# Kernel tuning notes

Hardware: AMD Instinct MI355X
Metric: run time of the kernel (lower is better)

The kernel has to match this reference:

```python
import jax, jax.numpy as jnp
import numpy as np

DIM = 1024
INNER = int(DIM * 1.5)
EPS = 1e-6


def setup_inputs() -> dict:
    key = jax.random.key(0)
    ks = jax.random.split(key, 8)
    B, L, D = 4, 2048, DIM
    s1 = 1.0 / np.sqrt(D)
    s2 = 1.0 / np.sqrt(INNER)
    return {
        "x": jax.random.normal(ks[0], (B, L, D), jnp.float32),
        "W1": jax.random.normal(ks[1], (D, INNER), jnp.float32) * s1,
        "b1": jnp.zeros((INNER,), jnp.float32),
        "W2": jax.random.normal(ks[2], (INNER, 3 * D), jnp.float32) * s2,
        "b2": jnp.zeros((3 * D,), jnp.float32),
        "Wv": jax.random.normal(ks[3], (D, D), jnp.float32) * (0.5 * s1),
        "bv": jnp.zeros((D,), jnp.float32),
        "mix_weight": jnp.full((D,), 0.5, jnp.float32),
        "norm_weight": jnp.ones((D,), jnp.float32),
    }


def rmsnorm(x, w):
    norm = jnp.sqrt(jnp.mean(x * x, axis=-1, keepdims=True) + EPS)
    return x / norm * w


def reference(x, W1, b1, W2, b2, Wv, bv, mix_weight, norm_weight):
    B, L, D = x.shape
    h = jax.nn.silu(x @ W1 + b1)              # [B,L,inner]
    qkg = h @ W2 + b2                          # [B,L,3D]
    q, k, g = jnp.split(qkg, 3, axis=-1)
    scores = jnp.einsum('bld,bmd->blm', q, k) / jnp.sqrt(jnp.float32(D))
    attn = jax.nn.softmax(scores, axis=-1)
    v = (x @ Wv + bv) * jax.nn.sigmoid(g)      # gated values [B,L,D]
    global_info = jnp.einsum('blm,bmd->bld', attn, v)
    output = mix_weight * global_info + (1.0 - mix_weight) * x
    return rmsnorm(output, norm_weight)
```

## Files before the change

kernel.cpp:

```cpp
#include <hip/hip_runtime.h>
#include <hip/hip_bf16.h>
#include <stdint.h>


typedef __bf16 bf16x8 __attribute__((ext_vector_type(8)));
typedef float f32x4 __attribute__((ext_vector_type(4)));

__device__ __forceinline__ unsigned short f2bf(float f) {
    unsigned int u = __float_as_uint(f);
    u += 0x7fffu + ((u >> 16) & 1u);
    return (unsigned short)(u >> 16);
}
__device__ __forceinline__ float bf2f(unsigned short s) {
    return __uint_as_float(((unsigned int)s) << 16);
}
__device__ __forceinline__ void llds16(const void* g, void* l) {
    __builtin_amdgcn_global_load_lds(
        (const __attribute__((address_space(1))) void*)g,
        (__attribute__((address_space(3))) void*)l, 16, 0, 0);
}

__global__ __launch_bounds__(256) void cvt_f32_bf16(
    const float* __restrict__ in, unsigned short* __restrict__ out, long long n8) {
    long long i = (long long)blockIdx.x * 256 + threadIdx.x;
    if (i >= n8) return;
    float4 a = ((const float4*)in)[2 * i];
    float4 b = ((const float4*)in)[2 * i + 1];
    ushort4 p0, p1;
    p0.x = f2bf(a.x); p0.y = f2bf(a.y); p0.z = f2bf(a.z); p0.w = f2bf(a.w);
    p1.x = f2bf(b.x); p1.y = f2bf(b.y); p1.z = f2bf(b.z); p1.w = f2bf(b.w);
    ((ushort4*)out)[2 * i] = p0;
    ((ushort4*)out)[2 * i + 1] = p1;
}

__global__ __launch_bounds__(256) void transpose_cvt(
    const float* __restrict__ in, unsigned short* __restrict__ out, int R, int C) {
    __shared__ unsigned short tile[32][33];
    int c0 = blockIdx.x * 32, r0 = blockIdx.y * 32;
    int cc = threadIdx.x & 31, rr = threadIdx.x >> 5;
#pragma unroll
    for (int p = 0; p < 4; ++p) {
        int r = rr + p * 8;
        tile[r][cc] = f2bf(in[(size_t)(r0 + r) * C + c0 + cc]);
    }
    __syncthreads();
#pragma unroll
    for (int p = 0; p < 4; ++p) {
        int c = rr + p * 8;
        out[(size_t)(c0 + c) * R + r0 + cc] = tile[cc][c];
    }
}

__global__ __launch_bounds__(256) void transpose_v(
    const unsigned short* __restrict__ in, unsigned short* __restrict__ out) {
    __shared__ unsigned short tile[32][33];
    int d0 = blockIdx.x * 32, m0 = blockIdx.y * 32;
    int cc = threadIdx.x & 31, rr = threadIdx.x >> 5;
#pragma unroll
    for (int p = 0; p < 4; ++p) {
        int r = rr + p * 8;
        tile[r][cc] = in[(size_t)(m0 + r) * 1024 + d0 + cc];
    }
    __syncthreads();
    int b = m0 >> 11, l0 = m0 & 2047;
#pragma unroll
    for (int p = 0; p < 4; ++p) {
        int d = rr + p * 8;
        out[((size_t)b * 1024 + d0 + d) * 2048 + l0 + cc] = tile[cc][d];
    }
}

template <int EPI>
__global__ __launch_bounds__(256, 3) void gemmk(
    const unsigned short* __restrict__ A, int lda, long long Abs,
    const unsigned short* __restrict__ B, int ldb, long long Bbs,
    int K,
    void* __restrict__ out, int ldo, long long Obs,
    const float* __restrict__ bias,
    const unsigned short* __restrict__ gate, int ldg,
    const float* __restrict__ xres, const float* __restrict__ mix,
    float scale, int gx) {
    __shared__ unsigned short lds[24576];
    const int tid = threadIdx.x, lane = tid & 63, wid = tid >> 6;
    const int nwg = gridDim.x;
    const int bswz = ((int)blockIdx.x & 7) * (nwg >> 3) + ((int)blockIdx.x >> 3);
    const int bx = bswz % gx, by = bswz / gx;
    const int bm = by * 128, bn = bx * 128;
    const int z = blockIdx.z;
    A += (long long)z * Abs;
    B += (long long)z * Bbs;
    const int NT = K >> 5;

    const int srow = tid >> 2;
    const int sswz = ((tid & 3) ^ ((tid >> 3) & 3)) * 8;
    size_t ag[2], bg[2];
    ag[0] = (size_t)(bm + srow) * lda + sswz;
    ag[1] = (size_t)(bm + 64 + srow) * lda + sswz;
    bg[0] = (size_t)(bn + srow) * ldb + sswz;
    bg[1] = (size_t)(bn + 64 + srow) * ldb + sswz;
    const int wl = wid * 512;

    auto stage = [&](int t, int bb) {
        const size_t k0 = (size_t)t << 5;
        llds16(A + ag[0] + k0, &lds[bb + wl]);
        llds16(A + ag[1] + k0, &lds[bb + 2048 + wl]);
        llds16(B + bg[0] + k0, &lds[bb + 4096 + wl]);
        llds16(B + bg[1] + k0, &lds[bb + 6144 + wl]);
    };

    const int wr = wid >> 1, wc = wid & 1;
    const int l15 = lane & 15, g4 = lane >> 4;
    const int fswz = (g4 ^ ((l15 >> 1) & 3)) * 8;
    const int aoff = (wr * 64 + l15) * 32 + fswz;
    const int boff = 4096 + (wc * 64 + l15) * 32 + fswz;

    f32x4 acc[4][4] = {};

    stage(0, 0);
    stage(1, 8192);
    asm volatile("s_waitcnt vmcnt(4)" ::: "memory");
    __builtin_amdgcn_s_barrier();

    int bb = 0;
    for (int t = 0; t < NT; ++t) {
        const bool st = (t + 2) < NT;
        if (st) {
            const int tgt = (bb >= 8192) ? bb - 8192 : bb + 16384;
            stage(t + 2, tgt);
        }
        __builtin_amdgcn_sched_barrier(0);
        bf16x8 af[4], bf[4];
#pragma unroll
        for (int i = 0; i < 4; ++i) {
            af[i] = *(const bf16x8*)&lds[bb + aoff + i * 512];
            bf[i] = *(const bf16x8*)&lds[bb + boff + i * 512];
        }
#pragma unroll
        for (int i = 0; i < 4; ++i)
#pragma unroll
            for (int j = 0; j < 4; ++j)
                acc[i][j] = __builtin_amdgcn_mfma_f32_16x16x32_bf16(
                    af[i], bf[j], acc[i][j], 0, 0, 0);
        asm volatile("s_waitcnt lgkmcnt(0)" ::: "memory");
        if (st) asm volatile("s_waitcnt vmcnt(4)" ::: "memory");
        else    asm volatile("s_waitcnt vmcnt(0)" ::: "memory");
        __builtin_amdgcn_s_barrier();
        bb = (bb == 16384) ? 0 : bb + 8192;
    }

    const int row0 = bm + wr * 64, col0 = bn + wc * 64;
#pragma unroll
    for (int i = 0; i < 4; ++i) {
#pragma unroll
        for (int j = 0; j < 4; ++j) {
            const int n = col0 + j * 16 + l15;
            const int mb = row0 + i * 16 + g4 * 4;
            f32x4 v = acc[i][j];
            if constexpr (EPI == 0 || EPI == 1) {
                float bs = bias[n];
                unsigned short* o = (unsigned short*)out;
#pragma unroll
                for (int q = 0; q < 4; ++q) {
                    float val = v[q] + bs;
                    if constexpr (EPI == 0) val = val / (1.f + __expf(-val));
                    o[(size_t)(mb + q) * ldo + n] = f2bf(val);
                }
            } else if constexpr (EPI == 2) {
                float bs = bias[n];
                unsigned short* o = (unsigned short*)out;
#pragma unroll
                for (int q = 0; q < 4; ++q) {
                    int m = mb + q;
                    float g = bf2f(gate[(size_t)m * ldg + n]);
                    float val = (v[q] + bs) / (1.f + __expf(-g));
                    o[(size_t)m * ldo + n] = f2bf(val);
                }
            } else if constexpr (EPI == 3) {
                float* o = (float*)out + (size_t)z * Obs;
#pragma unroll
                for (int q = 0; q < 4; ++q)
                    o[(size_t)(mb + q) * ldo + n] = v[q] * scale;
            } else {
                float* o = (float*)out + (size_t)z * Obs;
                const float* xr = xres + (size_t)z * Obs;
                float mw = mix[n];
#pragma unroll
                for (int q = 0; q < 4; ++q)
                    o[(size_t)(mb + q) * ldo + n] =
                        mw * v[q] + (1.f - mw) * xr[(size_t)(mb + q) * ldo + n];
            }
        }
    }
}

__global__ __launch_bounds__(256) void softmax_inplace(float* __restrict__ scores) {
    const int L = 2048;
    float* sr = scores + (size_t)blockIdx.x * L;
    const int t = threadIdx.x, lane = t & 63, wid = t >> 6;
    float4 a = ((const float4*)sr)[2 * t];
    float4 b = ((const float4*)sr)[2 * t + 1];
    float vv[8] = {a.x, a.y, a.z, a.w, b.x, b.y, b.z, b.w};
    float mx = vv[0];
#pragma unroll
    for (int i = 1; i < 8; ++i) mx = fmaxf(mx, vv[i]);
#pragma unroll
    for (int off = 32; off; off >>= 1) mx = fmaxf(mx, __shfl_xor(mx, off));
    __shared__ float redm[4], reds[4];
    if (lane == 0) redm[wid] = mx;
    __syncthreads();
    mx = fmaxf(fmaxf(redm[0], redm[1]), fmaxf(redm[2], redm[3]));
    float s = 0.f;
#pragma unroll
    for (int i = 0; i < 8; ++i) {
        vv[i] = __expf(vv[i] - mx);
        s += vv[i];
    }
#pragma unroll
    for (int off = 32; off; off >>= 1) s += __shfl_xor(s, off);
    if (lane == 0) reds[wid] = s;
    __syncthreads();
    s = reds[0] + reds[1] + reds[2] + reds[3];
    float inv = 1.f / s;
    ushort4 p0, p1;
    unsigned short* pp0 = (unsigned short*)&p0;
    unsigned short* pp1 = (unsigned short*)&p1;
#pragma unroll
    for (int i = 0; i < 4; ++i) pp0[i] = f2bf(vv[i] * inv);
#pragma unroll
    for (int i = 0; i < 4; ++i) pp1[i] = f2bf(vv[4 + i] * inv);
    unsigned short* pr = (unsigned short*)sr;
    ((ushort4*)pr)[2 * t] = p0;
    ((ushort4*)pr)[2 * t + 1] = p1;
}

__global__ __launch_bounds__(256) void rmsnorm_inplace(
    float* __restrict__ io, const float* __restrict__ w) {
    const int D = 1024;
    float* r = io + (size_t)blockIdx.x * D;
    const int t = threadIdx.x, lane = t & 63, wid = t >> 6;
    float4 v = ((const float4*)r)[t];
    float ss = v.x * v.x + v.y * v.y + v.z * v.z + v.w * v.w;
#pragma unroll
    for (int off = 32; off; off >>= 1) ss += __shfl_xor(ss, off);
    __shared__ float red[4];
    if (lane == 0) red[wid] = ss;
    __syncthreads();
    ss = red[0] + red[1] + red[2] + red[3];
    float sc = rsqrtf(ss / (float)D + 1e-6f);
    float4 wv = ((const float4*)w)[t];
    v.x *= sc * wv.x; v.y *= sc * wv.y; v.z *= sc * wv.z; v.w *= sc * wv.w;
    ((float4*)r)[t] = v;
}

extern "C" void kernel_launch(void* const* d_in, const int* in_sizes, int n_in,
                              void* d_out, int out_size, void* d_ws, size_t ws_size,
                              hipStream_t stream) {
    const float* x = (const float*)d_in[0];
    const float* W1 = (const float*)d_in[1];
    const float* b1 = (const float*)d_in[2];
    const float* W2 = (const float*)d_in[3];
    const float* b2 = (const float*)d_in[4];
    const float* Wv = (const float*)d_in[5];
    const float* bv = (const float*)d_in[6];
    const float* mixw = (const float*)d_in[7];
    const float* normw = (const float*)d_in[8];
    float* out = (float*)d_out;

    const int L = 2048, D = 1024, INNER = 1536, BN4 = 4;
    const int M = BN4 * L;

    char* w = (char*)d_ws;
    auto carve = [&](size_t bytes) {
        void* p = (void*)w;
        w += (bytes + 255) & ~(size_t)255;
        return p;
    };
    unsigned short* xbf = (unsigned short*)carve((size_t)M * D * 2);
    unsigned short* w1t = (unsigned short*)carve((size_t)INNER * D * 2);
    unsigned short* w2t = (unsigned short*)carve((size_t)3 * D * INNER * 2);
    unsigned short* wvt = (unsigned short*)carve((size_t)D * D * 2);
    unsigned short* h = (unsigned short*)carve((size_t)M * INNER * 2);
    unsigned short* qkg = (unsigned short*)carve((size_t)M * 3 * D * 2);
    unsigned short* vt = (unsigned short*)carve((size_t)BN4 * D * L * 2);
    float* scores = (float*)carve((size_t)BN4 * L * L * 4);
    unsigned short* vtmp = (unsigned short*)scores;

    cvt_f32_bf16<<<(M * D) / 2048, 256, 0, stream>>>(x, xbf, (long long)M * D / 8);
    transpose_cvt<<<dim3(INNER / 32, D / 32), 256, 0, stream>>>(W1, w1t, D, INNER);
    transpose_cvt<<<dim3(3 * D / 32, INNER / 32), 256, 0, stream>>>(W2, w2t, INNER, 3 * D);
    transpose_cvt<<<dim3(D / 32, D / 32), 256, 0, stream>>>(Wv, wvt, D, D);
    gemmk<0><<<dim3(768, 1, 1), 256, 0, stream>>>(
        xbf, D, 0, w1t, D, 0, D, h, INNER, 0, b1, nullptr, 0, nullptr, nullptr,
        1.f, 12);
    gemmk<1><<<dim3(1536, 1, 1), 256, 0, stream>>>(
        h, INNER, 0, w2t, INNER, 0, INNER, qkg, 3 * D, 0, b2, nullptr, 0, nullptr,
        nullptr, 1.f, 24);
    gemmk<2><<<dim3(512, 1, 1), 256, 0, stream>>>(
        xbf, D, 0, wvt, D, 0, D, vtmp, D, 0, bv, qkg + 2 * D, 3 * D, nullptr,
        nullptr, 1.f, 8);
    transpose_v<<<dim3(D / 32, M / 32), 256, 0, stream>>>(vtmp, vt);
    gemmk<3><<<dim3(256, 1, BN4), 256, 0, stream>>>(
        qkg, 3 * D, (long long)L * 3 * D, qkg + D, 3 * D, (long long)L * 3 * D, D,
        scores, L, (long long)L * L, nullptr, nullptr, 0, nullptr, nullptr,
        0.03125f, 16);
    softmax_inplace<<<BN4 * L, 256, 0, stream>>>(scores);
    gemmk<4><<<dim3(128, 1, BN4), 256, 0, stream>>>(
        (const unsigned short*)scores, 2 * L, (long long)L * 2 * L, vt, L,
        (long long)D * L, L, out, D, (long long)L * D, nullptr, nullptr, 0, x,
        mixw, 1.f, 8);
    rmsnorm_inplace<<<M, 256, 0, stream>>>(out, normw);
}
```

Measured before the change: 324.5 us.

## Add 256x128 8-wave GEMM with interleaved half-tile pipeline and fused V transpose

Adds a new GEMM kernel with 512 threads and 256x128 tiles at K-step 64. It double-buffers LDS and stages the A halves and the B tile at different points so that global-to-LDS loads overlap MFMA work, and it raises wave priority around the MFMA blocks. The QKG, V, score and PV GEMMs now use this kernel. The V-projection epilogue writes the transposed layout directly, which removes the separate transpose_v kernel and its intermediate buffer. The larger tiles cut redundant operand loads, but there are fewer workgroups, one block per CU, and more LDS per block.

```diff
diff --git a/kernel.cpp b/kernel.cpp
--- a/kernel.cpp
+++ b/kernel.cpp
@@ -5,6 +5,13 @@
 
 typedef __bf16 bf16x8 __attribute__((ext_vector_type(8)));
 typedef float f32x4 __attribute__((ext_vector_type(4)));
+
+#define VM4 asm volatile("s_waitcnt vmcnt(4)" ::: "memory")
+#define VM2 asm volatile("s_waitcnt vmcnt(2)" ::: "memory")
+#define VM0 asm volatile("s_waitcnt vmcnt(0)" ::: "memory")
+#define LGKM0 asm volatile("s_waitcnt lgkmcnt(0)" ::: "memory")
+#define BAR __builtin_amdgcn_s_barrier()
+#define SCB __builtin_amdgcn_sched_barrier(0)
 
 __device__ __forceinline__ unsigned short f2bf(float f) {
     unsigned int u = __float_as_uint(f);
@@ -18,6 +25,9 @@
     __builtin_amdgcn_global_load_lds(
         (const __attribute__((address_space(1))) void*)g,
         (__attribute__((address_space(3))) void*)l, 16, 0, 0);
+}
+__device__ __forceinline__ f32x4 MF(bf16x8 a, bf16x8 b, f32x4 c) {
+    return __builtin_amdgcn_mfma_f32_16x16x32_bf16(a, b, c, 0, 0, 0);
 }
 
 __global__ __launch_bounds__(256) void cvt_f32_bf16(
@@ -51,27 +61,8 @@
     }
 }
 
-__global__ __launch_bounds__(256) void transpose_v(
-    const unsigned short* __restrict__ in, unsigned short* __restrict__ out) {
-    __shared__ unsigned short tile[32][33];
-    int d0 = blockIdx.x * 32, m0 = blockIdx.y * 32;
-    int cc = threadIdx.x & 31, rr = threadIdx.x >> 5;
-#pragma unroll
-    for (int p = 0; p < 4; ++p) {
-        int r = rr + p * 8;
-        tile[r][cc] = in[(size_t)(m0 + r) * 1024 + d0 + cc];
-    }
-    __syncthreads();
-    int b = m0 >> 11, l0 = m0 & 2047;
-#pragma unroll
-    for (int p = 0; p < 4; ++p) {
-        int d = rr + p * 8;
-        out[((size_t)b * 1024 + d0 + d) * 2048 + l0 + cc] = tile[cc][d];
-    }
-}
-
 template <int EPI>
-__global__ __launch_bounds__(256, 3) void gemmk(
+__global__ __launch_bounds__(512, 1) void gemm5(
     const unsigned short* __restrict__ A, int lda, long long Abs,
     const unsigned short* __restrict__ B, int ldb, long long Bbs,
     int K,
@@ -80,15 +71,204 @@
     const unsigned short* __restrict__ gate, int ldg,
     const float* __restrict__ xres, const float* __restrict__ mix,
     float scale, int gx) {
+    __shared__ unsigned short lds[49152];
+    const int tid = threadIdx.x, lane = tid & 63, wid = tid >> 6;
+    const int wr = wid >> 1, wc = wid & 1;
+    const int nwg = gridDim.x;
+    const int bswz = ((int)blockIdx.x & 7) * (nwg >> 3) + ((int)blockIdx.x >> 3);
+    const int bx = bswz % gx, by = bswz / gx;
+    const int bm = by * 256, bn = bx * 128;
+    const int z = blockIdx.z;
+    A += (long long)z * Abs;
+    B += (long long)z * Bbs;
+    const int NT = K >> 6;
+
+    const int sswz = ((tid & 7) ^ ((tid >> 3) & 7)) * 8;
+    size_t agc[4], bgc[2];
+#pragma unroll
+    for (int c = 0; c < 4; ++c)
+        agc[c] = (size_t)(bm + c * 64 + (tid >> 3)) * lda + sswz;
+#pragma unroll
+    for (int c = 0; c < 2; ++c)
+        bgc[c] = (size_t)(bn + c * 64 + (tid >> 3)) * ldb + sswz;
+    const int wl = wid * 512;
+
+    auto stA01 = [&](int t, int buf) {
+        const size_t k0 = (size_t)t << 6;
+        llds16(A + agc[0] + k0, &lds[buf + wl]);
+        llds16(A + agc[1] + k0, &lds[buf + 4096 + wl]);
+    };
+    auto stA23 = [&](int t, int buf) {
+        const size_t k0 = (size_t)t << 6;
+        llds16(A + agc[2] + k0, &lds[buf + 8192 + wl]);
+        llds16(A + agc[3] + k0, &lds[buf + 12288 + wl]);
+    };
+    auto stB = [&](int t, int buf) {
+        const size_t k0 = (size_t)t << 6;
+        llds16(B + bgc[0] + k0, &lds[buf + 16384 + wl]);
+        llds16(B + bgc[1] + k0, &lds[buf + 20480 + wl]);
+    };
+
+    const int l15 = lane & 15, g4 = lane >> 4, l7 = lane & 7;
+    const int x0 = (g4 ^ l7) * 8, x1 = ((4 + g4) ^ l7) * 8;
+    const int ab = (wr * 64 + l15) * 64;
+    const int bbv = 16384 + (wc * 64 + l15) * 64;
+    constexpr int X = 0, Y = 24576;
+
+    f32x4 acc[4][4] = {};
+
+    stB(0, X); stA01(0, X); stA23(0, X); stB(1, Y);
+    VM4;
+    BAR; SCB;
+
+    int t = 0;
+    while (true) {
+        const bool last = (t + 2) >= NT;
+        bf16x8 bf[4][2], af[2][2];
+#pragma unroll
+        for (int j = 0; j < 4; ++j) {
+            bf[j][0] = *(const bf16x8*)&lds[X + bbv + j * 1024 + x0];
+            bf[j][1] = *(const bf16x8*)&lds[X + bbv + j * 1024 + x1];
+        }
+#pragma unroll
+        for (int i = 0; i < 2; ++i) {
+            af[i][0] = *(const bf16x8*)&lds[X + ab + i * 1024 + x0];
+            af[i][1] = *(const bf16x8*)&lds[X + ab + i * 1024 + x1];
+        }
+        stA01(t + 1, Y);
+        LGKM0; SCB;
+        __builtin_amdgcn_s_setprio(1);
+#pragma unroll
+        for (int s = 0; s < 2; ++s)
+#pragma unroll
+            for (int i = 0; i < 2; ++i)
+#pragma unroll
+                for (int j = 0; j < 4; ++j)
+                    acc[i][j] = MF(af[i][s], bf[j][s], acc[i][j]);
+        __builtin_amdgcn_s_setprio(0);
+        VM4;
+        BAR; SCB;
+#pragma unroll
+        for (int i = 0; i < 2; ++i) {
+            af[i][0] = *(const bf16x8*)&lds[X + ab + (2 + i) * 1024 + x0];
+            af[i][1] = *(const bf16x8*)&lds[X + ab + (2 + i) * 1024 + x1];
+        }
+        stA23(t + 1, Y);
+        if (!last) stB(t + 2, X);
+        LGKM0; SCB;
+        __builtin_amdgcn_s_setprio(1);
+#pragma unroll
+        for (int s = 0; s < 2; ++s)
+#pragma unroll
+            for (int i = 0; i < 2; ++i)
+#pragma unroll
+                for (int j = 0; j < 4; ++j)
+                    acc[2 + i][j] = MF(af[i][s], bf[j][s], acc[2 + i][j]);
+        __builtin_amdgcn_s_setprio(0);
+        if (last) { VM2; } else { VM4; }
+        BAR; SCB;
+#pragma unroll
+        for (int j = 0; j < 4; ++j) {
+            bf[j][0] = *(const bf16x8*)&lds[Y + bbv + j * 1024 + x0];
+            bf[j][1] = *(const bf16x8*)&lds[Y + bbv + j * 1024 + x1];
+        }
+#pragma unroll
+        for (int i = 0; i < 2; ++i) {
+            af[i][0] = *(const bf16x8*)&lds[Y + ab + i * 1024 + x0];
+            af[i][1] = *(const bf16x8*)&lds[Y + ab + i * 1024 + x1];
+        }
+        if (!last) stA01(t + 2, X);
+        LGKM0; SCB;
+        __builtin_amdgcn_s_setprio(1);
+#pragma unroll
+        for (int s = 0; s < 2; ++s)
+#pragma unroll
+            for (int i = 0; i < 2; ++i)
+#pragma unroll
+                for (int j = 0; j < 4; ++j)
+                    acc[i][j] = MF(af[i][s], bf[j][s], acc[i][j]);
+        __builtin_amdgcn_s_setprio(0);
+        if (last) { VM0; } else { VM4; }
+        BAR; SCB;
+#pragma unroll
+        for (int i = 0; i < 2; ++i) {
+            af[i][0] = *(const bf16x8*)&lds[Y + ab + (2 + i) * 1024 + x0];
+            af[i][1] = *(const bf16x8*)&lds[Y + ab + (2 + i) * 1024 + x1];
+        }
+        if (!last) { stA23(t + 2, X); stB(t + 3, Y); }
+        LGKM0; SCB;
+        __builtin_amdgcn_s_setprio(1);
+#pragma unroll
+        for (int s = 0; s < 2; ++s)
+#pragma unroll
+            for (int i = 0; i < 2; ++i)
+#pragma unroll
+                for (int j = 0; j < 4; ++j)
+                    acc[2 + i][j] = MF(af[i][s], bf[j][s], acc[2 + i][j]);
+        __builtin_amdgcn_s_setprio(0);
+        if (last) break;
+        VM4;
+        BAR; SCB;
+        t += 2;
+    }
+
+    const int row0 = bm + wr * 64, col0 = bn + wc * 64;
+#pragma unroll
+    for (int i = 0; i < 4; ++i) {
+#pragma unroll
+        for (int j = 0; j < 4; ++j) {
+            const int n = col0 + j * 16 + l15;
+            const int mb = row0 + i * 16 + g4 * 4;
+            f32x4 v = acc[i][j];
+            if constexpr (EPI == 1) {
+                float bs = bias[n];
+                unsigned short* o = (unsigned short*)out;
+#pragma unroll
+                for (int q = 0; q < 4; ++q)
+                    o[(size_t)(mb + q) * ldo + n] = f2bf(v[q] + bs);
+            } else if constexpr (EPI == 2) {
+                float bs = bias[n];
+                ushort4 pk;
+                unsigned short* pku = (unsigned short*)&pk;
+#pragma unroll
+                for (int q = 0; q < 4; ++q) {
+                    int m = mb + q;
+                    float g = bf2f(gate[(size_t)m * ldg + n]);
+                    pku[q] = f2bf((v[q] + bs) / (1.f + __expf(-g)));
+                }
+                unsigned short* o = (unsigned short*)out;
+                size_t oi = ((size_t)(mb >> 11) * 1024 + n) * 2048 + (mb & 2047);
+                *(ushort4*)(o + oi) = pk;
+            } else if constexpr (EPI == 3) {
+                float* o = (float*)out + (size_t)z * Obs;
+#pragma unroll
+                for (int q = 0; q < 4; ++q)
+                    o[(size_t)(mb + q) * ldo + n] = v[q] * scale;
+            } else {
+                float* o = (float*)out + (size_t)z * Obs;
+                const float* xr = xres + (size_t)z * Obs;
+                float mw = mix[n];
+#pragma unroll
+                for (int q = 0; q < 4; ++q)
+                    o[(size_t)(mb + q) * ldo + n] =
+                        mw * v[q] + (1.f - mw) * xr[(size_t)(mb + q) * ldo + n];
+            }
+        }
+    }
+}
+
+template <int EPI>
+__global__ __launch_bounds__(256, 3) void gemmk(
+    const unsigned short* __restrict__ A, int lda,
+    const unsigned short* __restrict__ B, int ldb,
+    int K, void* __restrict__ out, int ldo,
+    const float* __restrict__ bias, int gx) {
     __shared__ unsigned short lds[24576];
     const int tid = threadIdx.x, lane = tid & 63, wid = tid >> 6;
     const int nwg = gridDim.x;
     const int bswz = ((int)blockIdx.x & 7) * (nwg >> 3) + ((int)blockIdx.x >> 3);
     const int bx = bswz % gx, by = bswz / gx;
     const int bm = by * 128, bn = bx * 128;
-    const int z = blockIdx.z;
-    A += (long long)z * Abs;
-    B += (long long)z * Bbs;
     const int NT = K >> 5;
 
     const int srow = tid >> 2;
@@ -115,11 +295,9 @@
     const int boff = 4096 + (wc * 64 + l15) * 32 + fswz;
 
     f32x4 acc[4][4] = {};
-
     stage(0, 0);
     stage(1, 8192);
-    asm volatile("s_waitcnt vmcnt(4)" ::: "memory");
-    __builtin_amdgcn_s_barrier();
+    VM4; BAR;
 
     int bb = 0;
     for (int t = 0; t < NT; ++t) {
@@ -128,7 +306,7 @@
             const int tgt = (bb >= 8192) ? bb - 8192 : bb + 16384;
             stage(t + 2, tgt);
         }
-        __builtin_amdgcn_sched_barrier(0);
+        SCB;
         bf16x8 af[4], bf[4];
 #pragma unroll
         for (int i = 0; i < 4; ++i) {
@@ -139,12 +317,10 @@
         for (int i = 0; i < 4; ++i)
 #pragma unroll
             for (int j = 0; j < 4; ++j)
-                acc[i][j] = __builtin_amdgcn_mfma_f32_16x16x32_bf16(
-                    af[i], bf[j], acc[i][j], 0, 0, 0);
-        asm volatile("s_waitcnt lgkmcnt(0)" ::: "memory");
-        if (st) asm volatile("s_waitcnt vmcnt(4)" ::: "memory");
-        else    asm volatile("s_waitcnt vmcnt(0)" ::: "memory");
-        __builtin_amdgcn_s_barrier();
+                acc[i][j] = MF(af[i], bf[j], acc[i][j]);
+        LGKM0;
+        if (st) { VM4; } else { VM0; }
+        BAR;
         bb = (bb == 16384) ? 0 : bb + 8192;
     }
 
@@ -156,38 +332,13 @@
             const int n = col0 + j * 16 + l15;
             const int mb = row0 + i * 16 + g4 * 4;
             f32x4 v = acc[i][j];
-            if constexpr (EPI == 0 || EPI == 1) {
-                float bs = bias[n];
-                unsigned short* o = (unsigned short*)out;
-#pragma unroll
-                for (int q = 0; q < 4; ++q) {
-                    float val = v[q] + bs;
-                    if constexpr (EPI == 0) val = val / (1.f + __expf(-val));
-                    o[(size_t)(mb + q) * ldo + n] = f2bf(val);
-                }
-            } else if constexpr (EPI == 2) {
-                float bs = bias[n];
-                unsigned short* o = (unsigned short*)out;
-#pragma unroll
-                for (int q = 0; q < 4; ++q) {
-                    int m = mb + q;
-                    float g = bf2f(gate[(size_t)m * ldg + n]);
-                    float val = (v[q] + bs) / (1.f + __expf(-g));
-                    o[(size_t)m * ldo + n] = f2bf(val);
-                }
-            } else if constexpr (EPI == 3) {
-                float* o = (float*)out + (size_t)z * Obs;
-#pragma unroll
-                for (int q = 0; q < 4; ++q)
-                    o[(size_t)(mb + q) * ldo + n] = v[q] * scale;
-            } else {
-                float* o = (float*)out + (size_t)z * Obs;
-                const float* xr = xres + (size_t)z * Obs;
-                float mw = mix[n];
-#pragma unroll
-                for (int q = 0; q < 4; ++q)
-                    o[(size_t)(mb + q) * ldo + n] =
-                        mw * v[q] + (1.f - mw) * xr[(size_t)(mb + q) * ldo + n];
+            float bs = bias[n];
+            unsigned short* o = (unsigned short*)out;
+#pragma unroll
+            for (int q = 0; q < 4; ++q) {
+                float val = v[q] + bs;
+                if constexpr (EPI == 0) val = val / (1.f + __expf(-val));
+                o[(size_t)(mb + q) * ldo + n] = f2bf(val);
             }
         }
     }
@@ -283,28 +434,25 @@
     unsigned short* qkg = (unsigned short*)carve((size_t)M * 3 * D * 2);
     unsigned short* vt = (unsigned short*)carve((size_t)BN4 * D * L * 2);
     float* scores = (float*)carve((size_t)BN4 * L * L * 4);
-    unsigned short* vtmp = (unsigned short*)scores;
 
     cvt_f32_bf16<<<(M * D) / 2048, 256, 0, stream>>>(x, xbf, (long long)M * D / 8);
     transpose_cvt<<<dim3(INNER / 32, D / 32), 256, 0, stream>>>(W1, w1t, D, INNER);
     transpose_cvt<<<dim3(3 * D / 32, INNER / 32), 256, 0, stream>>>(W2, w2t, INNER, 3 * D);
     transpose_cvt<<<dim3(D / 32, D / 32), 256, 0, stream>>>(Wv, wvt, D, D);
-    gemmk<0><<<dim3(768, 1, 1), 256, 0, stream>>>(
-        xbf, D, 0, w1t, D, 0, D, h, INNER, 0, b1, nullptr, 0, nullptr, nullptr,
-        1.f, 12);
-    gemmk<1><<<dim3(1536, 1, 1), 256, 0, stream>>>(
-        h, INNER, 0, w2t, INNER, 0, INNER, qkg, 3 * D, 0, b2, nullptr, 0, nullptr,
-        nullptr, 1.f, 24);
-    gemmk<2><<<dim3(512, 1, 1), 256, 0, stream>>>(
-        xbf, D, 0, wvt, D, 0, D, vtmp, D, 0, bv, qkg + 2 * D, 3 * D, nullptr,
+    gemmk<0><<<dim3(768, 1, 1), 256, 0, stream>>>(xbf, D, w1t, D, D, h, INNER,
+                                                  b1, 12);
+    gemm5<1><<<dim3(768, 1, 1), 512, 0, stream>>>(
+        h, INNER, 0, w2t, INNER, 0, INNER, qkg, 3 * D, 0, b2, nullptr, 0,
+        nullptr, nullptr, 1.f, 24);
+    gemm5<2><<<dim3(256, 1, 1), 512, 0, stream>>>(
+        xbf, D, 0, wvt, D, 0, D, vt, L, 0, bv, qkg + 2 * D, 3 * D, nullptr,
         nullptr, 1.f, 8);
-    transpose_v<<<dim3(D / 32, M / 32), 256, 0, stream>>>(vtmp, vt);
-    gemmk<3><<<dim3(256, 1, BN4), 256, 0, stream>>>(
-        qkg, 3 * D, (long long)L * 3 * D, qkg + D, 3 * D, (long long)L * 3 * D, D,
-        scores, L, (long long)L * L, nullptr, nullptr, 0, nullptr, nullptr,
+    gemm5<3><<<dim3(128, 1, BN4), 512, 0, stream>>>(
+        qkg, 3 * D, (long long)L * 3 * D, qkg + D, 3 * D, (long long)L * 3 * D,
+        D, scores, L, (long long)L * L, nullptr, nullptr, 0, nullptr, nullptr,
         0.03125f, 16);
     softmax_inplace<<<BN4 * L, 256, 0, stream>>>(scores);
-    gemmk<4><<<dim3(128, 1, BN4), 256, 0, stream>>>(
+    gemm5<4><<<dim3(64, 1, BN4), 512, 0, stream>>>(
         (const unsigned short*)scores, 2 * L, (long long)L * 2 * L, vt, L,
         (long long)D * L, L, out, D, (long long)L * D, nullptr, nullptr, 0, x,
         mixw, 1.f, 8);
```

Result: faster. 291.1 us (-10.3%).
